# Optimization experiments

Measured on AMD Instinct MI355X. Metric: run time of the kernel, lower is better.

Reference implementation:

```python
import jax, jax.numpy as jnp
import numpy as np

B, L, D_MODEL = 4, 2048, 1024
D_INNER, D_STATE, D_CONV = 2 * D_MODEL, 16, 4
DT_RANK = (D_MODEL + 15) // 16  # 64


def silu(v):
    return v * jax.nn.sigmoid(v)


def setup_inputs() -> dict:
    key = jax.random.key(0)
    ks = jax.random.split(key, 8)
    n = lambda k, shape, s: jax.random.normal(k, shape, jnp.float32) * s
    A = jnp.broadcast_to(jnp.arange(1, D_STATE + 1, dtype=jnp.float32), (D_INNER, D_STATE))
    return {
        "x": jax.random.normal(ks[0], (B, L, D_MODEL), jnp.float32),
        "in_proj_w": n(ks[1], (2 * D_INNER, D_MODEL), 0.02),
        "conv_w": n(ks[2], (D_INNER, 1, D_CONV), 0.1),
        "conv_b": jnp.zeros((D_INNER,), jnp.float32),
        "x_proj_w": n(ks[3], (DT_RANK + 2 * D_STATE, D_INNER), 0.02),
        "dt_proj_w": n(ks[4], (D_INNER, DT_RANK), 0.1),
        "dt_proj_b": n(ks[5], (D_INNER,), 0.1),
        "A_log": jnp.log(A),
        "D": jnp.ones((D_INNER,), jnp.float32),
        "out_proj_w": n(ks[6], (D_MODEL, D_INNER), 0.02),
        "ln_g": jnp.ones((D_MODEL,), jnp.float32),
        "ln_b": jnp.zeros((D_MODEL,), jnp.float32),
    }


def mamba(x, in_proj_w, conv_w, conv_b, x_proj_w, dt_proj_w, dt_proj_b, A_log, D, out_proj_w):
    # in_proj -> (B, L, 2*d_inner), split into x-branch and gate z
    xz = jnp.einsum("bld,ed->ble", x, in_proj_w)
    xm, z = jnp.split(xz, 2, axis=-1)
    # depthwise causal conv over time
    xc = jnp.swapaxes(xm, 1, 2)  # (B, d_inner, L)
    xc = jax.lax.conv_general_dilated(
        xc, conv_w, (1,), [(D_CONV - 1, 0)],
        dimension_numbers=("NCH", "OIH", "NCH"), feature_group_count=D_INNER,
    ) + conv_b[None, :, None]
    xm = silu(jnp.swapaxes(xc, 1, 2))  # (B, L, d_inner)
    # input-dependent dt, B, C
    dbc = jnp.einsum("bld,ed->ble", xm, x_proj_w)
    dt, Bm, Cm = jnp.split(dbc, [DT_RANK, DT_RANK + D_STATE], axis=-1)
    dt = jax.nn.softplus(jnp.einsum("blr,dr->bld", dt, dt_proj_w) + dt_proj_b)
    A = -jnp.exp(A_log)  # (d_inner, d_state)

    def step(h, inp):
        dt_t, B_t, C_t, x_t = inp  # (B,d_inner),(B,d_state),(B,d_state),(B,d_inner)
        h = jnp.exp(dt_t[..., None] * A) * h + (dt_t * x_t)[..., None] * B_t[:, None, :]
        y = jnp.einsum("bds,bs->bd", h, C_t)
        return h, y

    h0 = jnp.zeros((B, D_INNER, D_STATE), xm.dtype)
    xs = (jnp.swapaxes(dt, 0, 1), jnp.swapaxes(Bm, 0, 1), jnp.swapaxes(Cm, 0, 1), jnp.swapaxes(xm, 0, 1))
    _, ys = jax.lax.scan(step, h0, xs)
    y = jnp.swapaxes(ys, 0, 1) + D * xm  # (B, L, d_inner)
    y = y * silu(z)
    return jnp.einsum("bld,od->blo", y, out_proj_w)


def layer_norm(h, g, b, eps=1e-5):
    mu = jnp.mean(h, axis=-1, keepdims=True)
    var = jnp.mean(jnp.square(h - mu), axis=-1, keepdims=True)
    return (h - mu) * jax.lax.rsqrt(var + eps) * g + b


def reference(x, in_proj_w, conv_w, conv_b, x_proj_w, dt_proj_w, dt_proj_b, A_log, D, out_proj_w, ln_g, ln_b):
    y = mamba(x, in_proj_w, conv_w, conv_b, x_proj_w, dt_proj_w, dt_proj_b, A_log, D, out_proj_w)
    # dropout_level=0 (eval): identity
    return layer_norm(y + x, ln_g, ln_b)
```

## Files before the change

kernel.cpp:

```cpp
#include <hip/hip_runtime.h>
#include <hip/hip_bf16.h>

#define B_ 4
#define L_ 2048
#define DM 1024
#define DI 2048
#define DSTATE 16
#define DTR 64
#define LC 64
#define NC (L_ / LC)
#define LOG2E 1.44269504f

typedef unsigned short ushort_t;
typedef __bf16 bf16x8 __attribute__((ext_vector_type(8)));
typedef float f32x4 __attribute__((ext_vector_type(4)));
typedef float f32x16 __attribute__((ext_vector_type(16)));
typedef unsigned short u16x8 __attribute__((ext_vector_type(8)));
typedef unsigned short u16x4 __attribute__((ext_vector_type(4)));

__device__ __forceinline__ ushort_t f2bf(float f) {
    unsigned u = __builtin_bit_cast(unsigned, f);
    unsigned r = (u + 0x7FFFu + ((u >> 16) & 1u)) >> 16;
    return (ushort_t)r;
}
__device__ __forceinline__ float bf2f(ushort_t h) {
    unsigned u = ((unsigned)h) << 16;
    return __builtin_bit_cast(float, u);
}

#define CV_E0 1048576
#define CV_E1 (CV_E0 + 49152)
#define CV_E2 (CV_E1 + 32768)
#define CV_E3 (CV_E2 + 524288)
#define CV_E4 (CV_E3 + 2097152)
__global__ __launch_bounds__(256) void k_cvt5(
    const float* __restrict__ s0, ushort_t* __restrict__ d0,
    const float* __restrict__ s1, ushort_t* __restrict__ d1,
    const float* __restrict__ s2, ushort_t* __restrict__ d2,
    const float* __restrict__ s3, ushort_t* __restrict__ d3,
    const float* __restrict__ s4, ushort_t* __restrict__ d4) {
    int g = blockIdx.x * 256 + threadIdx.x;
    const float* s;
    ushort_t* dst;
    int i;
    if (g < CV_E0)      { s = s0; dst = d0; i = g * 4; }
    else if (g < CV_E1) { s = s1; dst = d1; i = (g - CV_E0) * 4; }
    else if (g < CV_E2) { s = s2; dst = d2; i = (g - CV_E1) * 4; }
    else if (g < CV_E3) { s = s3; dst = d3; i = (g - CV_E2) * 4; }
    else                { s = s4; dst = d4; i = (g - CV_E3) * 4; }
    float4 v = *reinterpret_cast<const float4*>(s + i);
    ushort4 o;
    o.x = f2bf(v.x); o.y = f2bf(v.y); o.z = f2bf(v.z); o.w = f2bf(v.w);
    *reinterpret_cast<ushort4*>(dst + i) = o;
}

#define FENCE asm volatile("" ::: "memory")
#define VM8 asm volatile("s_waitcnt vmcnt(8)" ::: "memory")
#define VM4 asm volatile("s_waitcnt vmcnt(4)" ::: "memory")
#define VM0 asm volatile("s_waitcnt vmcnt(0)" ::: "memory")

__device__ __forceinline__ void mfma16(f32x4 acc[8][4], const bf16x8 av[4],
                                       const bf16x8 bv[4], int mh) {
#pragma unroll
    for (int i = 0; i < 4; ++i)
#pragma unroll
        for (int j = 0; j < 4; ++j)
            acc[mh * 4 + i][j] =
                __builtin_amdgcn_mfma_f32_16x16x32_bf16(av[i], bv[j], acc[mh * 4 + i][j], 0, 0, 0);
}

#define PHASE(BUF, MH, STAGE_STMT, WAIT_STMT)                                     \
    {                                                                             \
        bf16x8 av[4], bv[4];                                                      \
        _Pragma("unroll") for (int i_ = 0; i_ < 4; ++i_)                          \
            av[i_] = *(const bf16x8*)&lds[(BUF) * 16384 + aoff + ((MH) * 4 + i_) * 512]; \
        _Pragma("unroll") for (int i_ = 0; i_ < 4; ++i_)                          \
            bv[i_] = *(const bf16x8*)&lds[(BUF) * 16384 + boff + i_ * 512];       \
        STAGE_STMT;                                                               \
        FENCE; __builtin_amdgcn_s_barrier(); FENCE;                               \
        asm volatile("s_waitcnt lgkmcnt(0)" ::: "memory");                        \
        __builtin_amdgcn_sched_barrier(0);                                        \
        __builtin_amdgcn_s_setprio(1);                                            \
        mfma16(acc, av, bv, (MH));                                                \
        __builtin_amdgcn_s_setprio(0);                                            \
        WAIT_STMT;                                                                \
        FENCE; __builtin_amdgcn_s_barrier(); FENCE;                               \
    }

__global__ __launch_bounds__(512, 2) void k_gemm8(const ushort_t* __restrict__ Aq,
                                                  const ushort_t* __restrict__ Bq,
                                                  ushort_t* __restrict__ C) {
    __shared__ ushort_t lds[65536];
    const int tid = threadIdx.x;
    const int w = tid >> 6, lane = tid & 63;
    const int l15 = lane & 15;
    const int wm = w >> 2, wn = w & 3;
    const int bid = blockIdx.x;
    const int tm = (bid & 7) * 4 + ((bid >> 3) & 3);
    const int tn = bid >> 5;
    const int row0 = tm * 256, col0 = tn * 256;

    const int rs = w * 16 + (lane >> 2);
    const int lcs = (lane & 3) ^ ((lane >> 3) & 3);
    const int pcr = ((lane >> 4) ^ ((l15 >> 1) & 3)) * 8;
    const int aoff = wm * 4096 + l15 * 32 + pcr;
    const int boff = 8192 + (wn >> 1) * 4096 + (wn & 1) * 2048 + l15 * 32 + pcr;

    auto stA = [&](int buf, int t) {
        const ushort_t* s = Aq + (size_t)(row0 + rs) * 1024 + t * 32 + lcs * 8;
        __builtin_amdgcn_global_load_lds(
            (const __attribute__((address_space(1))) void*)s,
            (__attribute__((address_space(3))) void*)&lds[buf * 16384 + w * 512], 16, 0, 0);
        __builtin_amdgcn_global_load_lds(
            (const __attribute__((address_space(1))) void*)(s + 128 * 1024),
            (__attribute__((address_space(3))) void*)&lds[buf * 16384 + 4096 + w * 512], 16, 0, 0);
    };
    auto stB = [&](int buf, int t) {
        const ushort_t* s = Bq + (size_t)(col0 + rs) * 1024 + t * 32 + lcs * 8;
        __builtin_amdgcn_global_load_lds(
            (const __attribute__((address_space(1))) void*)s,
            (__attribute__((address_space(3))) void*)&lds[buf * 16384 + 8192 + w * 512], 16, 0, 0);
        __builtin_amdgcn_global_load_lds(
            (const __attribute__((address_space(1))) void*)(s + 128 * 1024),
            (__attribute__((address_space(3))) void*)&lds[buf * 16384 + 12288 + w * 512], 16, 0, 0);
    };

    f32x4 acc[8][4] = {};

    stA(0, 0); stB(0, 0);
    stA(1, 1); stB(1, 1);
    stA(2, 2); stB(2, 2);
    VM8;
    FENCE; __builtin_amdgcn_s_barrier(); FENCE;

#pragma unroll 1
    for (int k = 0; k < 7; ++k) {
        const int t3 = 4 * k + 3;
        PHASE(0, 0, stA(3, t3), (void)0);
        PHASE(0, 1, stB(3, t3), VM8);
        PHASE(1, 0, stA(0, t3 + 1), (void)0);
        PHASE(1, 1, stB(0, t3 + 1), VM8);
        PHASE(2, 0, stA(1, t3 + 2), (void)0);
        PHASE(2, 1, stB(1, t3 + 2), VM8);
        PHASE(3, 0, stA(2, t3 + 3), (void)0);
        PHASE(3, 1, stB(2, t3 + 3), VM8);
    }
    PHASE(0, 0, stA(3, 31), (void)0);
    PHASE(0, 1, stB(3, 31), VM8);
    PHASE(1, 0, (void)0, (void)0);
    PHASE(1, 1, (void)0, VM4);
    PHASE(2, 0, (void)0, (void)0);
    PHASE(2, 1, (void)0, VM0);
    PHASE(3, 0, (void)0, (void)0);
    PHASE(3, 1, (void)0, (void)0);

#pragma unroll
    for (int mf = 0; mf < 8; ++mf)
#pragma unroll
        for (int nf = 0; nf < 4; ++nf) {
            int col = col0 + wn * 64 + nf * 16 + l15;
#pragma unroll
            for (int r = 0; r < 4; ++r) {
                int row = row0 + wm * 128 + mf * 16 + (lane >> 4) * 4 + r;
                C[(size_t)row * 4096 + col] = f2bf(acc[mf][nf][r]);
            }
        }
}

template <int EPI, bool OUTBF>
__global__ __launch_bounds__(256) void k_gemm2(
    const ushort_t* __restrict__ A, const ushort_t* __restrict__ Bw,
    void* __restrict__ C, const float* __restrict__ bias,
    int M, int N, int K, int lda, int ldb, int ldc, int tilesM) {
    __shared__ ushort_t As[128 * 64];
    __shared__ ushort_t Bs[128 * 64];
    int tid = threadIdx.x;
    int lane = tid & 63, wv = tid >> 6;
    int wr = wv >> 1, wc = wv & 1;
    int bid = blockIdx.x;
    int tilesN = gridDim.x / tilesM;
    int per = 8 * tilesN;
    int grp = bid / per, within = bid % per;
    int tm = grp * 8 + (within & 7);
    int tn = within >> 3;
    int row0 = tm * 128, col0 = tn * 128;
    int kchunk = K / gridDim.z;
    int kbeg = blockIdx.z * kchunk, kend = kbeg + kchunk;
    float* Cf = (float*)C + (size_t)blockIdx.z * (size_t)M * ldc;

    int sr = lane >> 3;
    int sj = lane & 7;
    f32x4 acc[4][4] = {};

    for (int k0 = kbeg; k0 < kend; k0 += 64) {
        __syncthreads();
#pragma unroll
        for (int i = 0; i < 4; ++i) {
            int slot = wv * 4 + i;
            int r = slot * 8 + sr;
            int jA = sj ^ (r & 7);
            __builtin_amdgcn_global_load_lds(
                (const __attribute__((address_space(1))) void*)&A[(size_t)(row0 + r) * lda + k0 + jA * 8],
                (__attribute__((address_space(3))) void*)&As[slot * 512], 16, 0, 0);
            __builtin_amdgcn_global_load_lds(
                (const __attribute__((address_space(1))) void*)&Bw[(size_t)(col0 + r) * ldb + k0 + jA * 8],
                (__attribute__((address_space(3))) void*)&Bs[slot * 512], 16, 0, 0);
        }
        __syncthreads();
#pragma unroll
        for (int kk = 0; kk < 2; ++kk) {
            int co = kk * 32 + (lane >> 4) * 8;
            int sx = (lane & 7) << 3;
            bf16x8 af[4], bfr[4];
#pragma unroll
            for (int m = 0; m < 4; ++m) {
                int rw = wr * 64 + m * 16 + (lane & 15);
                af[m] = *reinterpret_cast<const bf16x8*>(&As[rw * 64 + (co ^ sx)]);
            }
#pragma unroll
            for (int n = 0; n < 4; ++n) {
                int rw = wc * 64 + n * 16 + (lane & 15);
                bfr[n] = *reinterpret_cast<const bf16x8*>(&Bs[rw * 64 + (co ^ sx)]);
            }
#pragma unroll
            for (int m = 0; m < 4; ++m)
#pragma unroll
                for (int n = 0; n < 4; ++n)
                    acc[m][n] = __builtin_amdgcn_mfma_f32_16x16x32_bf16(af[m], bfr[n], acc[m][n], 0, 0, 0);
        }
    }

#pragma unroll
    for (int m = 0; m < 4; ++m) {
#pragma unroll
        for (int n = 0; n < 4; ++n) {
            int col = col0 + wc * 64 + n * 16 + (lane & 15);
            if (col >= N) continue;
#pragma unroll
            for (int r = 0; r < 4; ++r) {
                int row = row0 + wr * 64 + m * 16 + (lane >> 4) * 4 + r;
                float v = acc[m][n][r];
                if (EPI == 1) {
                    v += bias[col];
                    v = (v > 20.f) ? v : log1pf(__expf(v));
                }
                if (OUTBF)
                    ((ushort_t*)C)[(size_t)row * ldc + col] = f2bf(v);
                else
                    Cf[(size_t)row * ldc + col] = v;
            }
        }
    }
}

__global__ __launch_bounds__(256) void k_red4(const float* __restrict__ p,
                                              ushort_t* __restrict__ o,
                                              int n, int stride) {
    int i = (blockIdx.x * 256 + threadIdx.x) * 4;
    if (i >= n) return;
    f32x4 a = *reinterpret_cast<const f32x4*>(&p[i]);
    f32x4 b = *reinterpret_cast<const f32x4*>(&p[i + stride]);
    f32x4 c = *reinterpret_cast<const f32x4*>(&p[i + 2 * stride]);
    f32x4 d = *reinterpret_cast<const f32x4*>(&p[i + 3 * stride]);
    ushort4 r;
    r.x = f2bf(a[0] + b[0] + c[0] + d[0]);
    r.y = f2bf(a[1] + b[1] + c[1] + d[1]);
    r.z = f2bf(a[2] + b[2] + c[2] + d[2]);
    r.w = f2bf(a[3] + b[3] + c[3] + d[3]);
    *reinterpret_cast<ushort4*>(&o[i]) = r;
}

__global__ __launch_bounds__(256) void k_conv(const ushort_t* __restrict__ xz,
                                              const float* __restrict__ w,
                                              const float* __restrict__ bias,
                                              ushort_t* __restrict__ out) {
    int d = blockIdx.x * 256 + threadIdx.x;
    int b = blockIdx.z;
    int t0 = blockIdx.y * 128;
    float w0 = w[d * 4 + 0], w1 = w[d * 4 + 1], w2 = w[d * 4 + 2], w3 = w[d * 4 + 3];
    float bi = bias[d];
    size_t base = ((size_t)b * L_) * (2 * DI) + d;
    size_t obase = ((size_t)b * L_) * DI + d;
    float x0 = (t0 >= 3) ? bf2f(xz[base + (size_t)(t0 - 3) * (2 * DI)]) : 0.f;
    float x1 = (t0 >= 2) ? bf2f(xz[base + (size_t)(t0 - 2) * (2 * DI)]) : 0.f;
    float x2 = (t0 >= 1) ? bf2f(xz[base + (size_t)(t0 - 1) * (2 * DI)]) : 0.f;
    for (int t = t0; t < t0 + 128; ++t) {
        float cur = bf2f(xz[base + (size_t)t * (2 * DI)]);
        float v = w0 * x0 + w1 * x1 + w2 * x2 + w3 * cur + bi;
        v = v / (1.f + __expf(-v));
        out[obase + (size_t)t * DI] = f2bf(v);
        x0 = x1; x1 = x2; x2 = cur;
    }
}


__global__ __launch_bounds__(256) void k_scan1(
    const ushort_t* __restrict__ dt, const ushort_t* __restrict__ xm,
    const ushort_t* __restrict__ dbc, const float* __restrict__ A_log,
    float* __restrict__ hfin, float* __restrict__ dtsum) {
    __shared__ float Bsh[LC][DSTATE];
    int tid = threadIdx.x;
    int d = blockIdx.x * 256 + tid;
    int c = blockIdx.y, b = blockIdx.z;
    f32x16 arow;
    float a1 = __expf(A_log[d * DSTATE]);
    bool ok = true;
#pragma unroll
    for (int s = 0; s < DSTATE; ++s) {
        float av = __expf(A_log[d * DSTATE + s]);
        arow[s] = -av * LOG2E;
        ok = ok && (fabsf(av - (float)(s + 1) * a1) <= 1e-4f * (float)(s + 1) * fabsf(a1) + 1e-6f);
    }
    float arow0 = -a1 * LOG2E;
    size_t rbase = (size_t)b * L_ + (size_t)c * LC;
    {
        int i = tid * 4;
        int t = i >> 4, s0 = i & 15;
        u16x4 v = *reinterpret_cast<const u16x4*>(&dbc[(rbase + t) * 96 + DTR + s0]);
#pragma unroll
        for (int j = 0; j < 4; ++j) Bsh[t][s0 + j] = bf2f(v[j]);
    }
    __syncthreads();
    f32x4 h0 = {}, h1 = {}, h2 = {}, h3 = {};
    float sd = 0.f;
    if (ok) {
        for (int t = 0; t < LC; ++t) {
            size_t ro = rbase + t;
            float dtv = bf2f(dt[ro * DI + d]);
            float xv = bf2f(xm[ro * DI + d]);
            float dx = dtv * xv;
            sd += dtv;
            float p = __builtin_amdgcn_exp2f(dtv * arow0);
            float p2 = p * p, p3 = p2 * p, p4 = p2 * p2;
            f32x4 ea = {p, p2, p3, p4};
            f32x4 eb = ea * p4, ec = eb * p4, ed = ec * p4;
            const f32x4* Bq = reinterpret_cast<const f32x4*>(&Bsh[t][0]);
            h0 = h0 * ea + Bq[0] * dx;
            h1 = h1 * eb + Bq[1] * dx;
            h2 = h2 * ec + Bq[2] * dx;
            h3 = h3 * ed + Bq[3] * dx;
        }
    } else {
        for (int t = 0; t < LC; ++t) {
            size_t ro = rbase + t;
            float dtv = bf2f(dt[ro * DI + d]);
            float xv = bf2f(xm[ro * DI + d]);
            float dx = dtv * xv;
            sd += dtv;
            const f32x4* Bq = reinterpret_cast<const f32x4*>(&Bsh[t][0]);
            f32x4 e0, e1, e2, e3;
#pragma unroll
            for (int j = 0; j < 4; ++j) {
                e0[j] = __builtin_amdgcn_exp2f(dtv * arow[j]);
                e1[j] = __builtin_amdgcn_exp2f(dtv * arow[4 + j]);
                e2[j] = __builtin_amdgcn_exp2f(dtv * arow[8 + j]);
                e3[j] = __builtin_amdgcn_exp2f(dtv * arow[12 + j]);
            }
            h0 = h0 * e0 + Bq[0] * dx;
            h1 = h1 * e1 + Bq[1] * dx;
            h2 = h2 * e2 + Bq[2] * dx;
            h3 = h3 * e3 + Bq[3] * dx;
        }
    }
    size_t hbase = (((size_t)b * NC + c) * DI + d) * DSTATE;
    *reinterpret_cast<f32x4*>(&hfin[hbase + 0]) = h0;
    *reinterpret_cast<f32x4*>(&hfin[hbase + 4]) = h1;
    *reinterpret_cast<f32x4*>(&hfin[hbase + 8]) = h2;
    *reinterpret_cast<f32x4*>(&hfin[hbase + 12]) = h3;
    dtsum[((size_t)b * NC + c) * DI + d] = sd;
}

__global__ __launch_bounds__(256) void k_scan2(
    float* __restrict__ hfin, const float* __restrict__ dtsum,
    const float* __restrict__ A_log) {
    int gid = blockIdx.x * 256 + threadIdx.x;
    int s = gid & (DSTATE - 1);
    int d = (gid >> 4) & (DI - 1);
    int b = gid >> 15;
    float Av = -__expf(A_log[d * DSTATE + s]) * LOG2E;
    float carry = 0.f;
    for (int c = 0; c < NC; ++c) {
        size_t idx = (((size_t)b * NC + c) * DI + d) * DSTATE + s;
        float loc = hfin[idx];
        hfin[idx] = carry;
        float sd = dtsum[((size_t)b * NC + c) * DI + d];
        carry = __builtin_amdgcn_exp2f(Av * sd) * carry + loc;
    }
}

__global__ __launch_bounds__(256) void k_scan3(
    const ushort_t* __restrict__ dt, const ushort_t* __restrict__ xm,
    const ushort_t* __restrict__ xz, const ushort_t* __restrict__ dbc,
    const float* __restrict__ A_log, const float* __restrict__ Dp,
    const float* __restrict__ hinit, ushort_t* __restrict__ yg) {
    __shared__ float Bsh[LC][DSTATE];
    __shared__ float Csh[LC][DSTATE];
    int tid = threadIdx.x;
    int d = blockIdx.x * 256 + tid;
    int c = blockIdx.y, b = blockIdx.z;
    f32x16 arow;
    float a1 = __expf(A_log[d * DSTATE]);
    bool ok = true;
#pragma unroll
    for (int s = 0; s < DSTATE; ++s) {
        float av = __expf(A_log[d * DSTATE + s]);
        arow[s] = -av * LOG2E;
        ok = ok && (fabsf(av - (float)(s + 1) * a1) <= 1e-4f * (float)(s + 1) * fabsf(a1) + 1e-6f);
    }
    float arow0 = -a1 * LOG2E;
    float Dd = Dp[d];
    size_t rbase = (size_t)b * L_ + (size_t)c * LC;
    {
        int e0 = tid * 8;
        int t = e0 >> 5, s0 = e0 & 31;
        u16x8 v = *reinterpret_cast<const u16x8*>(&dbc[(rbase + t) * 96 + DTR + s0]);
#pragma unroll
        for (int j = 0; j < 8; ++j) {
            int s = s0 + j;
            float f = bf2f(v[j]);
            if (s < DSTATE) Bsh[t][s] = f;
            else Csh[t][s - DSTATE] = f;
        }
    }
    __syncthreads();
    size_t hbase = (((size_t)b * NC + c) * DI + d) * DSTATE;
    f32x4 h0 = *reinterpret_cast<const f32x4*>(&hinit[hbase + 0]);
    f32x4 h1 = *reinterpret_cast<const f32x4*>(&hinit[hbase + 4]);
    f32x4 h2 = *reinterpret_cast<const f32x4*>(&hinit[hbase + 8]);
    f32x4 h3 = *reinterpret_cast<const f32x4*>(&hinit[hbase + 12]);
    if (ok) {
        for (int t = 0; t < LC; ++t) {
            size_t ro = rbase + t;
            float dtv = bf2f(dt[ro * DI + d]);
            float xv = bf2f(xm[ro * DI + d]);
            float zv = bf2f(xz[ro * (2 * DI) + DI + d]);
            float dx = dtv * xv;
            float p = __builtin_amdgcn_exp2f(dtv * arow0);
            float p2 = p * p, p3 = p2 * p, p4 = p2 * p2;
            f32x4 ea = {p, p2, p3, p4};
            f32x4 eb = ea * p4, ec = eb * p4, ed = ec * p4;
            const f32x4* Bq = reinterpret_cast<const f32x4*>(&Bsh[t][0]);
            const f32x4* Cq = reinterpret_cast<const f32x4*>(&Csh[t][0]);
            h0 = h0 * ea + Bq[0] * dx;
            h1 = h1 * eb + Bq[1] * dx;
            h2 = h2 * ec + Bq[2] * dx;
            h3 = h3 * ed + Bq[3] * dx;
            f32x4 y4 = h0 * Cq[0] + h1 * Cq[1] + h2 * Cq[2] + h3 * Cq[3];
            float y = (y4[0] + y4[1]) + (y4[2] + y4[3]) + Dd * xv;
            y *= zv / (1.f + __expf(-zv));
            yg[ro * DI + d] = f2bf(y);
        }
    } else {
        for (int t = 0; t < LC; ++t) {
            size_t ro = rbase + t;
            float dtv = bf2f(dt[ro * DI + d]);
            float xv = bf2f(xm[ro * DI + d]);
            float zv = bf2f(xz[ro * (2 * DI) + DI + d]);
            float dx = dtv * xv;
            const f32x4* Bq = reinterpret_cast<const f32x4*>(&Bsh[t][0]);
            const f32x4* Cq = reinterpret_cast<const f32x4*>(&Csh[t][0]);
            f32x4 e0, e1, e2, e3;
#pragma unroll
            for (int j = 0; j < 4; ++j) {
                e0[j] = __builtin_amdgcn_exp2f(dtv * arow[j]);
                e1[j] = __builtin_amdgcn_exp2f(dtv * arow[4 + j]);
                e2[j] = __builtin_amdgcn_exp2f(dtv * arow[8 + j]);
                e3[j] = __builtin_amdgcn_exp2f(dtv * arow[12 + j]);
            }
            h0 = h0 * e0 + Bq[0] * dx;
            h1 = h1 * e1 + Bq[1] * dx;
            h2 = h2 * e2 + Bq[2] * dx;
            h3 = h3 * e3 + Bq[3] * dx;
            f32x4 y4 = h0 * Cq[0] + h1 * Cq[1] + h2 * Cq[2] + h3 * Cq[3];
            float y = (y4[0] + y4[1]) + (y4[2] + y4[3]) + Dd * xv;
            y *= zv / (1.f + __expf(-zv));
            yg[ro * DI + d] = f2bf(y);
        }
    }
}

__global__ __launch_bounds__(256) void k_ln(const float* __restrict__ mo,
                                            const float* __restrict__ x,
                                            const float* __restrict__ g,
                                            const float* __restrict__ be,
                                            float* __restrict__ out) {
    __shared__ float red[8];
    size_t r = blockIdx.x;
    int tid = threadIdx.x;
    float4 hv = *reinterpret_cast<const float4*>(&mo[r * DM + tid * 4]);
    float4 xv = *reinterpret_cast<const float4*>(&x[r * DM + tid * 4]);
    float h0 = hv.x + xv.x, h1 = hv.y + xv.y, h2 = hv.z + xv.z, h3 = hv.w + xv.w;
    float s = h0 + h1 + h2 + h3;
    float q = h0 * h0 + h1 * h1 + h2 * h2 + h3 * h3;
#pragma unroll
    for (int o = 32; o > 0; o >>= 1) {
        s += __shfl_down(s, o);
        q += __shfl_down(q, o);
    }
    int lane = tid & 63, wid = tid >> 6;
    if (lane == 0) { red[wid] = s; red[4 + wid] = q; }
    __syncthreads();
    s = red[0] + red[1] + red[2] + red[3];
    q = red[4] + red[5] + red[6] + red[7];
    float mu = s * (1.f / DM);
    float var = q * (1.f / DM) - mu * mu;
    float rs = rsqrtf(var + 1e-5f);
    float4 gv = *reinterpret_cast<const float4*>(&g[tid * 4]);
    float4 bv = *reinterpret_cast<const float4*>(&be[tid * 4]);
    float4 o;
    o.x = (h0 - mu) * rs * gv.x + bv.x;
    o.y = (h1 - mu) * rs * gv.y + bv.y;
    o.z = (h2 - mu) * rs * gv.z + bv.z;
    o.w = (h3 - mu) * rs * gv.w + bv.w;
    *reinterpret_cast<float4*>(&out[r * DM + tid * 4]) = o;
}

extern "C" void kernel_launch(void* const* d_in, const int* in_sizes, int n_in,
                              void* d_out, int out_size, void* d_ws, size_t ws_size,
                              hipStream_t stream) {
    const float* x      = (const float*)d_in[0];
    const float* w_in   = (const float*)d_in[1];
    const float* conv_w = (const float*)d_in[2];
    const float* conv_b = (const float*)d_in[3];
    const float* w_xp   = (const float*)d_in[4];
    const float* w_dt   = (const float*)d_in[5];
    const float* dt_b   = (const float*)d_in[6];
    const float* A_log  = (const float*)d_in[7];
    const float* Dp     = (const float*)d_in[8];
    const float* w_out  = (const float*)d_in[9];
    const float* ln_g   = (const float*)d_in[10];
    const float* ln_b   = (const float*)d_in[11];
    float* out = (float*)d_out;

    char* ws = (char*)d_ws;
    size_t off = 0;
    auto alloc = [&](size_t bytes) -> void* {
        void* p = ws + off;
        off += (bytes + 255) & ~(size_t)255;
        return p;
    };
    const int M = B_ * L_;
    ushort_t* w_in_b  = (ushort_t*)alloc((size_t)2 * DI * DM * 2);
    ushort_t* w_xp_b  = (ushort_t*)alloc((size_t)96 * DI * 2);
    ushort_t* w_dt_b  = (ushort_t*)alloc((size_t)DI * DTR * 2);
    ushort_t* w_out_b = (ushort_t*)alloc((size_t)DM * DI * 2);
    ushort_t* x_b     = (ushort_t*)alloc((size_t)M * DM * 2);
    ushort_t* xz      = (ushort_t*)alloc((size_t)M * 2 * DI * 2);
    ushort_t* xm      = (ushort_t*)alloc((size_t)M * DI * 2);
    ushort_t* dbc     = (ushort_t*)alloc((size_t)M * 96 * 2);
    ushort_t* dtb     = (ushort_t*)alloc((size_t)M * DI * 2);
    ushort_t* yg      = (ushort_t*)alloc((size_t)M * DI * 2);
    float*    dtsum   = (float*)alloc((size_t)B_ * NC * DI * 4);
    float*    dbc_p   = (float*)alloc((size_t)4 * M * 96 * 4);
    float*    mo      = (float*)dtb;
    float*    hfin    = (float*)x_b;

    k_cvt5<<<dim3(CV_E4 / 256), 256, 0, stream>>>(
        w_in, w_in_b, w_xp, w_xp_b, w_dt, w_dt_b, w_out, w_out_b, x, x_b);

    k_gemm8<<<dim3(512), 512, 0, stream>>>(x_b, w_in_b, xz);
    k_conv<<<dim3(DI / 256, L_ / 128, B_), 256, 0, stream>>>(xz, conv_w, conv_b, xm);
    k_gemm2<0, false><<<dim3(64, 1, 4), 256, 0, stream>>>(
        xm, w_xp_b, dbc_p, nullptr, M, 96, DI, DI, DI, 96, 64);
    k_red4<<<dim3((M * 96 / 4 + 255) / 256), 256, 0, stream>>>(dbc_p, dbc, M * 96, M * 96);
    k_gemm2<1, true><<<dim3(64 * 16, 1, 1), 256, 0, stream>>>(
        dbc, w_dt_b, dtb, dt_b, M, DI, DTR, 96, DTR, DI, 64);
    k_scan1<<<dim3(DI / 256, NC, B_), 256, 0, stream>>>(dtb, xm, dbc, A_log, hfin, dtsum);
    k_scan2<<<dim3(B_ * DI * DSTATE / 256), 256, 0, stream>>>(hfin, dtsum, A_log);
    k_scan3<<<dim3(DI / 256, NC, B_), 256, 0, stream>>>(dtb, xm, xz, dbc, A_log, Dp, hfin, yg);
    k_gemm2<0, false><<<dim3(64 * 8, 1, 1), 256, 0, stream>>>(
        yg, w_out_b, mo, nullptr, M, DM, DI, DI, DI, DM, 64);
    k_ln<<<dim3(M), 256, 0, stream>>>(mo, x, ln_g, ln_b, out);
}
```

Baseline: 334.7 us.

## Replace out_proj GEMM with pipelined 256x128 MFMA kernel and bf16 output

Adds a dedicated out_proj GEMM kernel with 512 threads, 256x128 tiles, direct global-to-LDS loads and a four-buffer software pipeline, replacing the generic 128x128 GEMM. Its output is now written as bf16 instead of fp32, and the layer-norm kernel reads bf16. This targets better MFMA utilisation and less write/read traffic for the intermediate. The cost is reduced precision on the pre-residual output before LayerNorm, and only 256 blocks are launched.

```diff
diff --git a/kernel.cpp b/kernel.cpp
--- a/kernel.cpp
+++ b/kernel.cpp
@@ -56,7 +56,9 @@
 
 #define FENCE asm volatile("" ::: "memory")
 #define VM8 asm volatile("s_waitcnt vmcnt(8)" ::: "memory")
+#define VM6 asm volatile("s_waitcnt vmcnt(6)" ::: "memory")
 #define VM4 asm volatile("s_waitcnt vmcnt(4)" ::: "memory")
+#define VM3 asm volatile("s_waitcnt vmcnt(3)" ::: "memory")
 #define VM0 asm volatile("s_waitcnt vmcnt(0)" ::: "memory")
 
 __device__ __forceinline__ void mfma16(f32x4 acc[8][4], const bf16x8 av[4],
@@ -163,6 +165,92 @@
             for (int r = 0; r < 4; ++r) {
                 int row = row0 + wm * 128 + mf * 16 + (lane >> 4) * 4 + r;
                 C[(size_t)row * 4096 + col] = f2bf(acc[mf][nf][r]);
+            }
+        }
+}
+
+__global__ __launch_bounds__(512, 2) void k_gemm8o(const ushort_t* __restrict__ Aq,
+                                                   const ushort_t* __restrict__ Bq,
+                                                   ushort_t* __restrict__ C) {
+    __shared__ ushort_t lds[49152];
+    const int tid = threadIdx.x;
+    const int w = tid >> 6, lane = tid & 63;
+    const int l15 = lane & 15;
+    const int wm = w >> 2, wn = w & 3;
+    const int bid = blockIdx.x;
+    const int tm = bid & 31, tn = bid >> 5;
+    const int row0 = tm * 256, col0 = tn * 128;
+
+    const int rs = w * 16 + (lane >> 2);
+    const int lcs = (lane & 3) ^ ((lane >> 3) & 3);
+    const int pcr = ((lane >> 4) ^ ((l15 >> 1) & 3)) * 8;
+    const int aoff = wm * 4096 + l15 * 32 + pcr;
+    const int boff = 8192 + wn * 1024 + l15 * 32 + pcr;
+
+    auto stg = [&](int buf, int t) {
+        const ushort_t* sa = Aq + (size_t)(row0 + rs) * 2048 + t * 32 + lcs * 8;
+        __builtin_amdgcn_global_load_lds(
+            (const __attribute__((address_space(1))) void*)sa,
+            (__attribute__((address_space(3))) void*)&lds[buf * 12288 + w * 512], 16, 0, 0);
+        __builtin_amdgcn_global_load_lds(
+            (const __attribute__((address_space(1))) void*)(sa + 128 * 2048),
+            (__attribute__((address_space(3))) void*)&lds[buf * 12288 + 4096 + w * 512], 16, 0, 0);
+        const ushort_t* sb = Bq + (size_t)(col0 + rs) * 2048 + t * 32 + lcs * 8;
+        __builtin_amdgcn_global_load_lds(
+            (const __attribute__((address_space(1))) void*)sb,
+            (__attribute__((address_space(3))) void*)&lds[buf * 12288 + 8192 + w * 512], 16, 0, 0);
+    };
+
+    f32x4 acc[8][2] = {};
+
+#define OPHASE(BUF, STAGE_STMT, WAIT_STMT)                                        \
+    {                                                                             \
+        bf16x8 av[8], bv[2];                                                      \
+        _Pragma("unroll") for (int i_ = 0; i_ < 8; ++i_)                          \
+            av[i_] = *(const bf16x8*)&lds[(BUF) * 12288 + aoff + i_ * 512];       \
+        _Pragma("unroll") for (int i_ = 0; i_ < 2; ++i_)                          \
+            bv[i_] = *(const bf16x8*)&lds[(BUF) * 12288 + boff + i_ * 512];       \
+        STAGE_STMT;                                                               \
+        FENCE; __builtin_amdgcn_s_barrier(); FENCE;                               \
+        asm volatile("s_waitcnt lgkmcnt(0)" ::: "memory");                        \
+        __builtin_amdgcn_sched_barrier(0);                                        \
+        __builtin_amdgcn_s_setprio(1);                                            \
+        _Pragma("unroll") for (int i_ = 0; i_ < 8; ++i_)                          \
+            _Pragma("unroll") for (int j_ = 0; j_ < 2; ++j_)                      \
+                acc[i_][j_] = __builtin_amdgcn_mfma_f32_16x16x32_bf16(            \
+                    av[i_], bv[j_], acc[i_][j_], 0, 0, 0);                        \
+        __builtin_amdgcn_s_setprio(0);                                            \
+        WAIT_STMT;                                                                \
+        FENCE; __builtin_amdgcn_s_barrier(); FENCE;                               \
+    }
+
+    stg(0, 0); stg(1, 1); stg(2, 2);
+    VM6;
+    FENCE; __builtin_amdgcn_s_barrier(); FENCE;
+
+#pragma unroll 1
+    for (int k = 0; k < 15; ++k) {
+        const int t3 = 4 * k + 3;
+        OPHASE(0, stg(3, t3), VM6);
+        OPHASE(1, stg(0, t3 + 1), VM6);
+        OPHASE(2, stg(1, t3 + 2), VM6);
+        OPHASE(3, stg(2, t3 + 3), VM6);
+    }
+    OPHASE(0, stg(3, 63), VM6);
+    OPHASE(1, (void)0, VM3);
+    OPHASE(2, (void)0, VM0);
+    OPHASE(3, (void)0, (void)0);
+#undef OPHASE
+
+#pragma unroll
+    for (int mf = 0; mf < 8; ++mf)
+#pragma unroll
+        for (int nf = 0; nf < 2; ++nf) {
+            int col = col0 + wn * 32 + nf * 16 + l15;
+#pragma unroll
+            for (int r = 0; r < 4; ++r) {
+                int row = row0 + wm * 128 + mf * 16 + (lane >> 4) * 4 + r;
+                C[(size_t)row * 1024 + col] = f2bf(acc[mf][nf][r]);
             }
         }
 }
@@ -292,7 +380,6 @@
         x0 = x1; x1 = x2; x2 = cur;
     }
 }
-
 
 __global__ __launch_bounds__(256) void k_scan1(
     const ushort_t* __restrict__ dt, const ushort_t* __restrict__ xm,
@@ -479,7 +566,7 @@
     }
 }
 
-__global__ __launch_bounds__(256) void k_ln(const float* __restrict__ mo,
+__global__ __launch_bounds__(256) void k_ln(const ushort_t* __restrict__ mo,
                                             const float* __restrict__ x,
                                             const float* __restrict__ g,
                                             const float* __restrict__ be,
@@ -487,9 +574,10 @@
     __shared__ float red[8];
     size_t r = blockIdx.x;
     int tid = threadIdx.x;
-    float4 hv = *reinterpret_cast<const float4*>(&mo[r * DM + tid * 4]);
+    ushort4 mv = *reinterpret_cast<const ushort4*>(&mo[r * DM + tid * 4]);
     float4 xv = *reinterpret_cast<const float4*>(&x[r * DM + tid * 4]);
-    float h0 = hv.x + xv.x, h1 = hv.y + xv.y, h2 = hv.z + xv.z, h3 = hv.w + xv.w;
+    float h0 = bf2f(mv.x) + xv.x, h1 = bf2f(mv.y) + xv.y;
+    float h2 = bf2f(mv.z) + xv.z, h3 = bf2f(mv.w) + xv.w;
     float s = h0 + h1 + h2 + h3;
     float q = h0 * h0 + h1 * h1 + h2 * h2 + h3 * h3;
 #pragma unroll
@@ -552,7 +640,7 @@
     ushort_t* yg      = (ushort_t*)alloc((size_t)M * DI * 2);
     float*    dtsum   = (float*)alloc((size_t)B_ * NC * DI * 4);
     float*    dbc_p   = (float*)alloc((size_t)4 * M * 96 * 4);
-    float*    mo      = (float*)dtb;
+    ushort_t* mo      = dtb;
     float*    hfin    = (float*)x_b;
 
     k_cvt5<<<dim3(CV_E4 / 256), 256, 0, stream>>>(
@@ -568,7 +656,6 @@
     k_scan1<<<dim3(DI / 256, NC, B_), 256, 0, stream>>>(dtb, xm, dbc, A_log, hfin, dtsum);
     k_scan2<<<dim3(B_ * DI * DSTATE / 256), 256, 0, stream>>>(hfin, dtsum, A_log);
     k_scan3<<<dim3(DI / 256, NC, B_), 256, 0, stream>>>(dtb, xm, xz, dbc, A_log, Dp, hfin, yg);
-    k_gemm2<0, false><<<dim3(64 * 8, 1, 1), 256, 0, stream>>>(
-        yg, w_out_b, mo, nullptr, M, DM, DI, DI, DI, DM, 64);
+    k_gemm8o<<<dim3(256), 512, 0, stream>>>(yg, w_out_b, mo);
     k_ln<<<dim3(M), 256, 0, stream>>>(mo, x, ln_g, ln_b, out);
 }
```

After: 329.0 us. No clear change (-1.7%).

## Replace in-proj GEMM with templated 256x128 pipelined kernel and reuse for out-proj

Applied to the files above, without the earlier changes.

The 256x256 four-buffer in-projection GEMM becomes a templated 256x128 tile kernel with triple-buffered direct-to-LDS loads, using less shared memory and launching more blocks. The same kernel now runs the out-projection in place of the generic 128-tile GEMM, writing bf16 output that the layer norm converts back to float. This targets better occupancy and load balance plus a faster out-projection. In exchange, each tile does less reuse per load, and the out-projection result is rounded to bf16 before the residual add, costing some accuracy.

```diff
diff --git a/kernel.cpp b/kernel.cpp
--- a/kernel.cpp
+++ b/kernel.cpp
@@ -55,114 +55,96 @@
 }
 
 #define FENCE asm volatile("" ::: "memory")
-#define VM8 asm volatile("s_waitcnt vmcnt(8)" ::: "memory")
-#define VM4 asm volatile("s_waitcnt vmcnt(4)" ::: "memory")
+#define VM3 asm volatile("s_waitcnt vmcnt(3)" ::: "memory")
 #define VM0 asm volatile("s_waitcnt vmcnt(0)" ::: "memory")
 
-__device__ __forceinline__ void mfma16(f32x4 acc[8][4], const bf16x8 av[4],
-                                       const bf16x8 bv[4], int mh) {
-#pragma unroll
-    for (int i = 0; i < 4; ++i)
-#pragma unroll
-        for (int j = 0; j < 4; ++j)
-            acc[mh * 4 + i][j] =
-                __builtin_amdgcn_mfma_f32_16x16x32_bf16(av[i], bv[j], acc[mh * 4 + i][j], 0, 0, 0);
-}
-
-#define PHASE(BUF, MH, STAGE_STMT, WAIT_STMT)                                     \
+template <int KK, int LDC, int NT>
+__global__ __launch_bounds__(512, 2) void k_gemmP(const ushort_t* __restrict__ Aq,
+                                                  const ushort_t* __restrict__ Bq,
+                                                  ushort_t* __restrict__ C) {
+    __shared__ ushort_t lds[36864];
+    const int tid = threadIdx.x;
+    const int w = tid >> 6, lane = tid & 63;
+    const int l15 = lane & 15;
+    const int wm = w >> 2, wn = w & 3;
+    const int bid = blockIdx.x;
+    const int tm = bid & 31, tn = bid >> 5;
+    const int row0 = tm * 256, col0 = tn * 128;
+
+    const int rs = w * 16 + (lane >> 2);
+    const int lcs = (lane & 3) ^ ((lane >> 3) & 3);
+    const int pcr = ((lane >> 4) ^ ((l15 >> 1) & 3)) * 8;
+    const int aoff = wm * 4096 + l15 * 32 + pcr;
+    const int boff = 8192 + wn * 1024 + l15 * 32 + pcr;
+
+    auto stg = [&](int buf, int t) {
+        const ushort_t* sa = Aq + (size_t)(row0 + rs) * KK + t * 32 + lcs * 8;
+        __builtin_amdgcn_global_load_lds(
+            (const __attribute__((address_space(1))) void*)sa,
+            (__attribute__((address_space(3))) void*)&lds[buf * 12288 + w * 512], 16, 0, 0);
+        __builtin_amdgcn_global_load_lds(
+            (const __attribute__((address_space(1))) void*)(sa + (size_t)128 * KK),
+            (__attribute__((address_space(3))) void*)&lds[buf * 12288 + 4096 + w * 512], 16, 0, 0);
+        const ushort_t* sb = Bq + (size_t)(col0 + rs) * KK + t * 32 + lcs * 8;
+        __builtin_amdgcn_global_load_lds(
+            (const __attribute__((address_space(1))) void*)sb,
+            (__attribute__((address_space(3))) void*)&lds[buf * 12288 + 8192 + w * 512], 16, 0, 0);
+    };
+
+    f32x4 acc[8][2] = {};
+
+#define GPHASE(BUF, STAGE_STMT, WAIT_STMT)                                        \
     {                                                                             \
-        bf16x8 av[4], bv[4];                                                      \
-        _Pragma("unroll") for (int i_ = 0; i_ < 4; ++i_)                          \
-            av[i_] = *(const bf16x8*)&lds[(BUF) * 16384 + aoff + ((MH) * 4 + i_) * 512]; \
-        _Pragma("unroll") for (int i_ = 0; i_ < 4; ++i_)                          \
-            bv[i_] = *(const bf16x8*)&lds[(BUF) * 16384 + boff + i_ * 512];       \
+        bf16x8 av[8], bv[2];                                                      \
+        _Pragma("unroll") for (int i_ = 0; i_ < 8; ++i_)                          \
+            av[i_] = *(const bf16x8*)&lds[(BUF) * 12288 + aoff + i_ * 512];       \
+        _Pragma("unroll") for (int i_ = 0; i_ < 2; ++i_)                          \
+            bv[i_] = *(const bf16x8*)&lds[(BUF) * 12288 + boff + i_ * 512];       \
         STAGE_STMT;                                                               \
         FENCE; __builtin_amdgcn_s_barrier(); FENCE;                               \
         asm volatile("s_waitcnt lgkmcnt(0)" ::: "memory");                        \
         __builtin_amdgcn_sched_barrier(0);                                        \
         __builtin_amdgcn_s_setprio(1);                                            \
-        mfma16(acc, av, bv, (MH));                                                \
+        _Pragma("unroll") for (int i_ = 0; i_ < 8; ++i_)                          \
+            _Pragma("unroll") for (int j_ = 0; j_ < 2; ++j_)                      \
+                acc[i_][j_] = __builtin_amdgcn_mfma_f32_16x16x32_bf16(            \
+                    av[i_], bv[j_], acc[i_][j_], 0, 0, 0);                        \
         __builtin_amdgcn_s_setprio(0);                                            \
         WAIT_STMT;                                                                \
         FENCE; __builtin_amdgcn_s_barrier(); FENCE;                               \
     }
 
-__global__ __launch_bounds__(512, 2) void k_gemm8(const ushort_t* __restrict__ Aq,
-                                                  const ushort_t* __restrict__ Bq,
-                                                  ushort_t* __restrict__ C) {
-    __shared__ ushort_t lds[65536];
-    const int tid = threadIdx.x;
-    const int w = tid >> 6, lane = tid & 63;
-    const int l15 = lane & 15;
-    const int wm = w >> 2, wn = w & 3;
-    const int bid = blockIdx.x;
-    const int tm = (bid & 7) * 4 + ((bid >> 3) & 3);
-    const int tn = bid >> 5;
-    const int row0 = tm * 256, col0 = tn * 256;
-
-    const int rs = w * 16 + (lane >> 2);
-    const int lcs = (lane & 3) ^ ((lane >> 3) & 3);
-    const int pcr = ((lane >> 4) ^ ((l15 >> 1) & 3)) * 8;
-    const int aoff = wm * 4096 + l15 * 32 + pcr;
-    const int boff = 8192 + (wn >> 1) * 4096 + (wn & 1) * 2048 + l15 * 32 + pcr;
-
-    auto stA = [&](int buf, int t) {
-        const ushort_t* s = Aq + (size_t)(row0 + rs) * 1024 + t * 32 + lcs * 8;
-        __builtin_amdgcn_global_load_lds(
-            (const __attribute__((address_space(1))) void*)s,
-            (__attribute__((address_space(3))) void*)&lds[buf * 16384 + w * 512], 16, 0, 0);
-        __builtin_amdgcn_global_load_lds(
-            (const __attribute__((address_space(1))) void*)(s + 128 * 1024),
-            (__attribute__((address_space(3))) void*)&lds[buf * 16384 + 4096 + w * 512], 16, 0, 0);
-    };
-    auto stB = [&](int buf, int t) {
-        const ushort_t* s = Bq + (size_t)(col0 + rs) * 1024 + t * 32 + lcs * 8;
-        __builtin_amdgcn_global_load_lds(
-            (const __attribute__((address_space(1))) void*)s,
-            (__attribute__((address_space(3))) void*)&lds[buf * 16384 + 8192 + w * 512], 16, 0, 0);
-        __builtin_amdgcn_global_load_lds(
-            (const __attribute__((address_space(1))) void*)(s + 128 * 1024),
-            (__attribute__((address_space(3))) void*)&lds[buf * 16384 + 12288 + w * 512], 16, 0, 0);
-    };
-
-    f32x4 acc[8][4] = {};
-
-    stA(0, 0); stB(0, 0);
-    stA(1, 1); stB(1, 1);
-    stA(2, 2); stB(2, 2);
-    VM8;
+    stg(0, 0); stg(1, 1);
+    VM3;
     FENCE; __builtin_amdgcn_s_barrier(); FENCE;
 
 #pragma unroll 1
-    for (int k = 0; k < 7; ++k) {
-        const int t3 = 4 * k + 3;
-        PHASE(0, 0, stA(3, t3), (void)0);
-        PHASE(0, 1, stB(3, t3), VM8);
-        PHASE(1, 0, stA(0, t3 + 1), (void)0);
-        PHASE(1, 1, stB(0, t3 + 1), VM8);
-        PHASE(2, 0, stA(1, t3 + 2), (void)0);
-        PHASE(2, 1, stB(1, t3 + 2), VM8);
-        PHASE(3, 0, stA(2, t3 + 3), (void)0);
-        PHASE(3, 1, stB(2, t3 + 3), VM8);
-    }
-    PHASE(0, 0, stA(3, 31), (void)0);
-    PHASE(0, 1, stB(3, 31), VM8);
-    PHASE(1, 0, (void)0, (void)0);
-    PHASE(1, 1, (void)0, VM4);
-    PHASE(2, 0, (void)0, (void)0);
-    PHASE(2, 1, (void)0, VM0);
-    PHASE(3, 0, (void)0, (void)0);
-    PHASE(3, 1, (void)0, (void)0);
+    for (int k = 0; k < (NT - 2) / 3; ++k) {
+        const int t0 = 3 * k;
+        GPHASE(0, stg(2, t0 + 2), VM3);
+        GPHASE(1, stg(0, t0 + 3), VM3);
+        GPHASE(2, stg(1, t0 + 4), VM3);
+    }
+    if constexpr ((NT - 2) % 3 == 2) {
+        GPHASE(0, stg(2, NT - 2), VM3);
+        GPHASE(1, stg(0, NT - 1), VM3);
+        GPHASE(2, (void)0, VM0);
+        GPHASE(0, (void)0, (void)0);
+    } else {
+        GPHASE(0, (void)0, VM0);
+        GPHASE(1, (void)0, (void)0);
+    }
+#undef GPHASE
 
 #pragma unroll
     for (int mf = 0; mf < 8; ++mf)
 #pragma unroll
-        for (int nf = 0; nf < 4; ++nf) {
-            int col = col0 + wn * 64 + nf * 16 + l15;
+        for (int nf = 0; nf < 2; ++nf) {
+            int col = col0 + wn * 32 + nf * 16 + l15;
 #pragma unroll
             for (int r = 0; r < 4; ++r) {
                 int row = row0 + wm * 128 + mf * 16 + (lane >> 4) * 4 + r;
-                C[(size_t)row * 4096 + col] = f2bf(acc[mf][nf][r]);
+                C[(size_t)row * LDC + col] = f2bf(acc[mf][nf][r]);
             }
         }
 }
@@ -292,7 +274,6 @@
         x0 = x1; x1 = x2; x2 = cur;
     }
 }
-
 
 __global__ __launch_bounds__(256) void k_scan1(
     const ushort_t* __restrict__ dt, const ushort_t* __restrict__ xm,
@@ -479,7 +460,7 @@
     }
 }
 
-__global__ __launch_bounds__(256) void k_ln(const float* __restrict__ mo,
+__global__ __launch_bounds__(256) void k_ln(const ushort_t* __restrict__ mo,
                                             const float* __restrict__ x,
                                             const float* __restrict__ g,
                                             const float* __restrict__ be,
@@ -487,9 +468,10 @@
     __shared__ float red[8];
     size_t r = blockIdx.x;
     int tid = threadIdx.x;
-    float4 hv = *reinterpret_cast<const float4*>(&mo[r * DM + tid * 4]);
+    ushort4 mv = *reinterpret_cast<const ushort4*>(&mo[r * DM + tid * 4]);
     float4 xv = *reinterpret_cast<const float4*>(&x[r * DM + tid * 4]);
-    float h0 = hv.x + xv.x, h1 = hv.y + xv.y, h2 = hv.z + xv.z, h3 = hv.w + xv.w;
+    float h0 = bf2f(mv.x) + xv.x, h1 = bf2f(mv.y) + xv.y;
+    float h2 = bf2f(mv.z) + xv.z, h3 = bf2f(mv.w) + xv.w;
     float s = h0 + h1 + h2 + h3;
     float q = h0 * h0 + h1 * h1 + h2 * h2 + h3 * h3;
 #pragma unroll
@@ -552,13 +534,13 @@
     ushort_t* yg      = (ushort_t*)alloc((size_t)M * DI * 2);
     float*    dtsum   = (float*)alloc((size_t)B_ * NC * DI * 4);
     float*    dbc_p   = (float*)alloc((size_t)4 * M * 96 * 4);
-    float*    mo      = (float*)dtb;
+    ushort_t* mo      = dtb;
     float*    hfin    = (float*)x_b;
 
     k_cvt5<<<dim3(CV_E4 / 256), 256, 0, stream>>>(
         w_in, w_in_b, w_xp, w_xp_b, w_dt, w_dt_b, w_out, w_out_b, x, x_b);
 
-    k_gemm8<<<dim3(512), 512, 0, stream>>>(x_b, w_in_b, xz);
+    k_gemmP<1024, 4096, 32><<<dim3(1024), 512, 0, stream>>>(x_b, w_in_b, xz);
     k_conv<<<dim3(DI / 256, L_ / 128, B_), 256, 0, stream>>>(xz, conv_w, conv_b, xm);
     k_gemm2<0, false><<<dim3(64, 1, 4), 256, 0, stream>>>(
         xm, w_xp_b, dbc_p, nullptr, M, 96, DI, DI, DI, 96, 64);
@@ -568,7 +550,6 @@
     k_scan1<<<dim3(DI / 256, NC, B_), 256, 0, stream>>>(dtb, xm, dbc, A_log, hfin, dtsum);
     k_scan2<<<dim3(B_ * DI * DSTATE / 256), 256, 0, stream>>>(hfin, dtsum, A_log);
     k_scan3<<<dim3(DI / 256, NC, B_), 256, 0, stream>>>(dtb, xm, xz, dbc, A_log, Dp, hfin, yg);
-    k_gemm2<0, false><<<dim3(64 * 8, 1, 1), 256, 0, stream>>>(
-        yg, w_out_b, mo, nullptr, M, DM, DI, DI, DI, DM, 64);
+    k_gemmP<2048, 1024, 64><<<dim3(256), 512, 0, stream>>>(yg, w_out_b, mo);
     k_ln<<<dim3(M), 256, 0, stream>>>(mo, x, ln_g, ln_b, out);
 }
```

Result: no change. 330.0 us (-1.4%).
